# Optimization experiments

Measured on AMD Instinct MI355X. Metric: run time of the kernel, lower is better.

Reference implementation:

```python
import jax, jax.numpy as jnp
import numpy as np

NUM_HEADS = 16
NEG = -1e9


def setup_inputs() -> dict:
    key = jax.random.key(0)
    ks = jax.random.split(key, 16)
    B, Sq, Skv, E = 4, 4096, 4096, 1024
    scale = 1.0 / np.sqrt(E)
    inp = {
        "q": jax.random.normal(ks[0], (B, Sq, E), jnp.float32),
        "k": jax.random.normal(ks[1], (B, Skv, E), jnp.float32),
        "v": jax.random.normal(ks[2], (B, Skv, E), jnp.float32),
        "q_padding_mask": jax.random.randint(ks[3], (B, Sq, 1), 0, 2).astype(bool),
        "key_padding_mask": jax.random.randint(ks[4], (B, Skv, 1), 0, 2).astype(bool),
        "Wq": jax.random.normal(ks[5], (E, E), jnp.float32) * scale,
        "bq": jnp.zeros((E,), jnp.float32),
        "Wk": jax.random.normal(ks[6], (E, E), jnp.float32) * scale,
        "bk": jnp.zeros((E,), jnp.float32),
        "Wv": jax.random.normal(ks[7], (E, E), jnp.float32) * scale,
        "bv": jnp.zeros((E,), jnp.float32),
        "Wp": jax.random.normal(ks[8], (E, E), jnp.float32) * scale,
        "bp": jnp.zeros((E,), jnp.float32),
    }
    return inp


def _split_heads(x, H):
    B, S, E = x.shape
    return x.reshape(B, S, H, E // H).transpose(0, 2, 1, 3)  # (B,H,S,D)


def reference(q, k, v, q_padding_mask, key_padding_mask, Wq, bq, Wk, bk, Wv, bv, Wp, bp):
    B, Sq, E = q.shape
    H = NUM_HEADS
    # padding: q*mask + ~mask*(-1e9) == where(mask, q, -1e9)
    q = jnp.where(q_padding_mask, q, NEG)
    k = jnp.where(key_padding_mask, k, NEG)
    v = v * key_padding_mask
    # projections (torch nn.Linear: x @ W.T + b)
    qh = _split_heads(q @ Wq.T + bq, H)  # (B,H,Sq,D)
    kh = _split_heads(k @ Wk.T + bk, H)  # (B,H,Skv,D)
    vh = _split_heads(v @ Wv.T + bv, H)  # (B,H,Skv,D)
    qh = jax.nn.softmax(qh, axis=-1)
    kh = jax.nn.softmax(kh, axis=-1)
    k_cumsum = kh.sum(axis=-2, keepdims=True)              # (B,H,1,D)
    a_t = 1.0 / (qh * k_cumsum).sum(axis=-1, keepdims=True)  # (B,H,Sq,1)
    context = jnp.einsum("bhsd,bhse->bhde", kh, vh)        # (B,H,D,D)
    out = jnp.einsum("bhqd,bhde->bhqe", qh, context) * a_t + qh
    out = out.transpose(0, 2, 1, 3).reshape(B, Sq, E)
    out = out @ Wp.T + bp
    return out * q_padding_mask
```

## Files before the change

### kernel.cpp

```cpp
#include <hip/hip_runtime.h>
#include <hip/hip_bf16.h>
#include <stdint.h>


typedef __bf16 bf16_t;
typedef __bf16 v8bf __attribute__((ext_vector_type(8)));
typedef __bf16 v4bf __attribute__((ext_vector_type(4)));
typedef float  v4f  __attribute__((ext_vector_type(4)));

#define NSPLIT 16

__device__ __forceinline__ void gl_lds16(const void* g, void* l) {
  __builtin_amdgcn_global_load_lds((const __attribute__((address_space(1))) void*)g,
                                   (__attribute__((address_space(3))) void*)l,
                                   16, 0, 0);
}

__global__ __launch_bounds__(256) void convert_w(
    const float* __restrict__ W0, const float* __restrict__ W1,
    const float* __restrict__ W2, const float* __restrict__ W3,
    bf16_t* __restrict__ dst)
{
  int g = blockIdx.x * 256 + threadIdx.x;
  int seg = g >> 17;
  int off = (g & 131071) * 8;
  const float* s = (seg == 0 ? W0 : seg == 1 ? W1 : seg == 2 ? W2 : W3) + off;
  v4f a = *(const v4f*)s, b = *(const v4f*)(s + 4);
  v8bf o;
#pragma unroll
  for (int j = 0; j < 4; j++) { o[j] = (bf16_t)a[j]; o[4 + j] = (bf16_t)b[j]; }
  *(v8bf*)(dst + (size_t)seg * 1048576 + off) = o;
}

__device__ __forceinline__ void cvt_chunk(const float* __restrict__ s,
                                          bf16_t* __restrict__ d, size_t chunk)
{
  const size_t i = chunk * 8;
  v4f a = *(const v4f*)(s + i), b = *(const v4f*)(s + i + 4);
  v8bf o;
#pragma unroll
  for (int j = 0; j < 4; j++) { o[j] = (bf16_t)a[j]; o[4 + j] = (bf16_t)b[j]; }
  *(v8bf*)(d + i) = o;
}

__global__ __launch_bounds__(256) void convert_kv_kernel(
    const float* __restrict__ k, const float* __restrict__ v,
    bf16_t* __restrict__ kb, bf16_t* __restrict__ vb)
{
  const size_t t = (size_t)blockIdx.x * 256 + threadIdx.x;
#pragma unroll
  for (int j = 0; j < 4; j++) cvt_chunk(k, kb, t + (size_t)j * 524288);
#pragma unroll
  for (int j = 0; j < 4; j++) cvt_chunk(v, vb, t + (size_t)j * 524288);
}

__global__ __launch_bounds__(256) void convert_q_kernel(
    const float* __restrict__ q, bf16_t* __restrict__ qb)
{
  const size_t t = (size_t)blockIdx.x * 256 + threadIdx.x;
#pragma unroll
  for (int j = 0; j < 4; j++) cvt_chunk(q, qb, t + (size_t)j * 524288);
}

__global__ __launch_bounds__(256) void rowsum_kernel(
    const float* __restrict__ Wq, const float* __restrict__ bq,
    const float* __restrict__ Wk, const float* __restrict__ bk,
    float* __restrict__ rs)
{
  int w = threadIdx.x >> 6, l = threadIdx.x & 63;
  int row = blockIdx.x * 4 + w;
  int r = (row < 1024) ? row : row - 1024;
  const float* W = ((row < 1024) ? Wq : Wk) + (size_t)r * 1024 + l * 16;
  float s = 0.f;
#pragma unroll
  for (int i = 0; i < 4; i++) {
    v4f x = *(const v4f*)(W + i * 4);
    s += x[0] + x[1] + x[2] + x[3];
  }
#pragma unroll
  for (int sh = 1; sh < 64; sh <<= 1) s += __shfl_xor(s, sh, 64);
  if (l == 0) {
    float b = (row < 1024) ? bq[r] : bk[r];
    rs[row] = -1e9f * s + b;
  }
}

template <int EPI>
__global__ __launch_bounds__(512, 2) void gemm_bt(
    const bf16_t* __restrict__ A, const bf16_t* __restrict__ Wb,
    const float* __restrict__ bias, const int* __restrict__ rowmask,
    const float* __restrict__ rs, void* __restrict__ Cout)
{
  constexpr int K = 1024, N = 1024;
  constexpr int NT = 16;
  __shared__ __align__(16) bf16_t As[2][256 * 64];
  __shared__ __align__(16) bf16_t Bs[2][256 * 64];
  const int t = threadIdx.x;
  const int l = t & 63;
  const int w = t >> 6;
  const int wm = w >> 2, wn = w & 3;
  const int xcd = blockIdx.x & 7, seq = blockIdx.x >> 3;
  const int by = xcd * 8 + (seq & 7), bx = seq >> 3;
  const int m0 = by << 8, n0 = bx << 8;

  const int srow = t >> 3;
  const int sgs  = (t & 7) ^ (srow & 7);
  const bf16_t* Ag = A  + (size_t)(m0 + srow) * K + sgs * 8;
  const bf16_t* Bg = Wb + (size_t)(n0 + srow) * K + sgs * 8;
  bf16_t* lA = &As[0][0] + t * 8;
  bf16_t* lB = &Bs[0][0] + t * 8;

  auto stageA = [&](int half, int kt, int buf) {
    const bf16_t* s = Ag + (size_t)(half * 128) * K + (kt << 6);
    bf16_t* d = lA + buf * 16384 + half * 8192;
    gl_lds16(s, d);
    gl_lds16(s + (size_t)64 * K, d + 4096);
  };
  auto stageB = [&](int half, int kt, int buf) {
    const bf16_t* s = Bg + (size_t)(half * 128) * K + (kt << 6);
    bf16_t* d = lB + buf * 16384 + half * 8192;
    gl_lds16(s, d);
    gl_lds16(s + (size_t)64 * K, d + 4096);
  };

  const int lr = l & 15, kg = l >> 4;
  const int xg0 = ((kg)     ^ (lr & 7)) * 8;
  const int xg1 = ((4 + kg) ^ (lr & 7)) * 8;
  const int aB = (wm * 128 + lr) * 64;
  const int bB = (wn * 64  + lr) * 64;

  v4f acc[8][4] = {};
  v8bf bfr[4][2];

#define QUAD(R0, R1, A0_, A1_, A2_, A3_)                                        \
  {                                                                             \
    __builtin_amdgcn_s_setprio(1);                                              \
    _Pragma("unroll")                                                           \
    for (int c = 0; c < 4; ++c) {                                               \
      acc[R0][c] = __builtin_amdgcn_mfma_f32_16x16x32_bf16(A0_, bfr[c][0], acc[R0][c], 0, 0, 0); \
      acc[R0][c] = __builtin_amdgcn_mfma_f32_16x16x32_bf16(A1_, bfr[c][1], acc[R0][c], 0, 0, 0); \
      acc[R1][c] = __builtin_amdgcn_mfma_f32_16x16x32_bf16(A2_, bfr[c][0], acc[R1][c], 0, 0, 0); \
      acc[R1][c] = __builtin_amdgcn_mfma_f32_16x16x32_bf16(A3_, bfr[c][1], acc[R1][c], 0, 0, 0); \
    }                                                                           \
    __builtin_amdgcn_s_setprio(0);                                              \
  }

  stageA(0, 0, 0); stageA(1, 0, 0); stageB(0, 0, 0); stageB(1, 0, 0);
  stageB(0, 1, 1); stageB(1, 1, 1);
  asm volatile("s_waitcnt vmcnt(4)" ::: "memory");
  __builtin_amdgcn_s_barrier();

  for (int s = 0; s < NT; ++s) {
    const int b = s & 1;
    const bf16_t* Ab = &As[b][0];
    const bf16_t* Bb = &Bs[b][0];
    v8bf a0, a1, a2, a3;
#pragma unroll
    for (int c = 0; c < 4; ++c) {
      bfr[c][0] = *(const v8bf*)(Bb + bB + c * 1024 + xg0);
      bfr[c][1] = *(const v8bf*)(Bb + bB + c * 1024 + xg1);
    }
    a0 = *(const v8bf*)(Ab + aB + 0 * 1024 + xg0);
    a1 = *(const v8bf*)(Ab + aB + 0 * 1024 + xg1);
    a2 = *(const v8bf*)(Ab + aB + 1 * 1024 + xg0);
    a3 = *(const v8bf*)(Ab + aB + 1 * 1024 + xg1);
    if (s + 1 < NT) { stageA(0, s + 1, b ^ 1); stageA(1, s + 1, b ^ 1); }
    __builtin_amdgcn_s_barrier();
    QUAD(0, 1, a0, a1, a2, a3);
    __builtin_amdgcn_s_barrier();
    a0 = *(const v8bf*)(Ab + aB + 2 * 1024 + xg0);
    a1 = *(const v8bf*)(Ab + aB + 2 * 1024 + xg1);
    a2 = *(const v8bf*)(Ab + aB + 3 * 1024 + xg0);
    a3 = *(const v8bf*)(Ab + aB + 3 * 1024 + xg1);
    __builtin_amdgcn_s_barrier();
    QUAD(2, 3, a0, a1, a2, a3);
    __builtin_amdgcn_s_barrier();
    a0 = *(const v8bf*)(Ab + aB + 4 * 1024 + xg0);
    a1 = *(const v8bf*)(Ab + aB + 4 * 1024 + xg1);
    a2 = *(const v8bf*)(Ab + aB + 5 * 1024 + xg0);
    a3 = *(const v8bf*)(Ab + aB + 5 * 1024 + xg1);
    if (s + 2 < NT) { stageB(0, s + 2, b); stageB(1, s + 2, b); }
    __builtin_amdgcn_s_barrier();
    QUAD(4, 5, a0, a1, a2, a3);
    __builtin_amdgcn_s_barrier();
    a0 = *(const v8bf*)(Ab + aB + 6 * 1024 + xg0);
    a1 = *(const v8bf*)(Ab + aB + 6 * 1024 + xg1);
    a2 = *(const v8bf*)(Ab + aB + 7 * 1024 + xg0);
    a3 = *(const v8bf*)(Ab + aB + 7 * 1024 + xg1);
    __builtin_amdgcn_s_barrier();
    QUAD(6, 7, a0, a1, a2, a3);
    if (s < NT - 2) asm volatile("s_waitcnt vmcnt(4)" ::: "memory");
    else            asm volatile("s_waitcnt vmcnt(0)" ::: "memory");
    __builtin_amdgcn_s_barrier();
  }
#undef QUAD

  const int rq = kg * 4;
  float bcol[4], rscol[4]; int colg[4];
#pragma unroll
  for (int c = 0; c < 4; c++) {
    colg[c] = n0 + wn * 64 + c * 16 + lr;
    bcol[c] = bias[colg[c]];
    rscol[c] = (EPI == 1) ? rs[colg[c]] : 0.f;
  }
#pragma unroll
  for (int r = 0; r < 8; r++) {
    int rowBase = m0 + wm * 128 + r * 16 + rq;
#pragma unroll
    for (int i = 0; i < 4; i++) {
      int row = rowBase + i;
      int msk = rowmask[row];
      float vv[4];
#pragma unroll
      for (int c = 0; c < 4; c++) {
        float x = acc[r][c][i] + bcol[c];
        if (EPI == 0)      x = msk ? x : bcol[c];
        else if (EPI == 1) x = msk ? x : rscol[c];
        else               x = msk ? x : 0.f;
        vv[c] = x;
      }
      if (EPI == 1) {
        float mx = fmaxf(fmaxf(vv[0], vv[1]), fmaxf(vv[2], vv[3]));
#pragma unroll
        for (int sh = 1; sh < 16; sh <<= 1) mx = fmaxf(mx, __shfl_xor(mx, sh, 64));
        float e0 = __expf(vv[0] - mx), e1 = __expf(vv[1] - mx);
        float e2 = __expf(vv[2] - mx), e3 = __expf(vv[3] - mx);
        float sum = e0 + e1 + e2 + e3;
#pragma unroll
        for (int sh = 1; sh < 16; sh <<= 1) sum += __shfl_xor(sum, sh, 64);
        float rinv = 1.0f / sum;
        vv[0] = e0 * rinv; vv[1] = e1 * rinv; vv[2] = e2 * rinv; vv[3] = e3 * rinv;
      }
#pragma unroll
      for (int c = 0; c < 4; c++) {
        size_t idx = (size_t)row * N + colg[c];
        if (EPI == 2) ((float*)Cout)[idx] = vv[c];
        else          ((bf16_t*)Cout)[idx] = (bf16_t)vv[c];
      }
    }
  }
}

__global__ __launch_bounds__(256) void ctx_partial(
    const bf16_t* __restrict__ kh, const bf16_t* __restrict__ vh,
    float* __restrict__ ctx, float* __restrict__ kc)
{
  __shared__ __align__(16) float khTf[2][64][36];
  __shared__ __align__(16) float vhTf[2][64][36];
  const int bh = blockIdx.x & 63;
  const int sp = blockIdx.x >> 6;
  const int b = bh >> 4, h = bh & 15;
  const int t = threadIdx.x;
  const int l = t & 63;
  const int w = t >> 6;
  const int wm = w >> 1, wn = w & 1;

  const int a  = t & 7;
  const int d0 = a * 8;
  const int sl = t >> 3;
  const int sw = sl ^ (a << 2);

  const size_t base = ((size_t)b * 4096) * 1024 + h * 64;
  const int sBeg = sp * (4096 / NSPLIT);
  const int nch = (4096 / NSPLIT) / 32;
  const bf16_t* kp = kh + base + (size_t)(sBeg + sl) * 1024 + d0;
  const bf16_t* vp = vh + base + (size_t)(sBeg + sl) * 1024 + d0;

  const int lr = l & 15;
  const int gl = l >> 4;

  v8bf ones;
#pragma unroll
  for (int j = 0; j < 8; j++) ones[j] = (bf16_t)1.0f;

  v4f acc[2][2] = {};
  v4f kca[2] = {};

  auto loadfrag = [&](const float (*T)[36], int rowbase) -> v8bf {
    const int row = rowbase + lr;
    const float* rp = &T[row][0];
    const int g0 = ((gl << 1) ^ (row >> 3)) & 7;
    v4f pa = *(const v4f*)(rp + g0 * 4);
    v4f pb = *(const v4f*)(rp + (g0 ^ 1) * 4);
    v8bf f;
#pragma unroll
    for (int j = 0; j < 4; j++) { f[j] = (bf16_t)pa[j]; f[4 + j] = (bf16_t)pb[j]; }
    return f;
  };

  v8bf rk = *(const v8bf*)kp;
  v8bf rv = *(const v8bf*)vp;
  for (int c = 0; c < nch; c++) {
    const int cur = c & 1;
#pragma unroll
    for (int j = 0; j < 8; j++) {
      khTf[cur][d0 + j][sw] = (float)rk[j];
      vhTf[cur][d0 + j][sw] = (float)rv[j];
    }
    if (c + 1 < nch) {
      rk = *(const v8bf*)(kp + (size_t)(c + 1) * 32 * 1024);
      rv = *(const v8bf*)(vp + (size_t)(c + 1) * 32 * 1024);
    }
    __syncthreads();
    v8bf af0 = loadfrag(khTf[cur], wm * 32);
    v8bf af1 = loadfrag(khTf[cur], wm * 32 + 16);
    v8bf bf0 = loadfrag(vhTf[cur], wn * 32);
    v8bf bf1 = loadfrag(vhTf[cur], wn * 32 + 16);
    acc[0][0] = __builtin_amdgcn_mfma_f32_16x16x32_bf16(af0, bf0, acc[0][0], 0, 0, 0);
    acc[0][1] = __builtin_amdgcn_mfma_f32_16x16x32_bf16(af0, bf1, acc[0][1], 0, 0, 0);
    acc[1][0] = __builtin_amdgcn_mfma_f32_16x16x32_bf16(af1, bf0, acc[1][0], 0, 0, 0);
    acc[1][1] = __builtin_amdgcn_mfma_f32_16x16x32_bf16(af1, bf1, acc[1][1], 0, 0, 0);
    if (wn == 0) {
      kca[0] = __builtin_amdgcn_mfma_f32_16x16x32_bf16(af0, ones, kca[0], 0, 0, 0);
      kca[1] = __builtin_amdgcn_mfma_f32_16x16x32_bf16(af1, ones, kca[1], 0, 0, 0);
    }
    __syncthreads();
  }

  const int rq = gl * 4;
  float* cp = ctx + (size_t)bh * 4096;
#pragma unroll
  for (int r = 0; r < 2; r++)
#pragma unroll
    for (int cc = 0; cc < 2; cc++) {
      const int e = wn * 32 + cc * 16 + lr;
#pragma unroll
      for (int i = 0; i < 4; i++) {
        const int d = wm * 32 + r * 16 + rq + i;
        atomicAdd(&cp[d * 64 + e], acc[r][cc][i]);
      }
    }
  if (wn == 0 && lr == 0) {
#pragma unroll
    for (int r = 0; r < 2; r++)
#pragma unroll
      for (int i = 0; i < 4; i++) {
        const int d = wm * 32 + r * 16 + rq + i;
        atomicAdd(&kc[bh * 64 + d], kca[r][i]);
      }
  }
}

__global__ __launch_bounds__(256) void outpre_kernel(
    const bf16_t* __restrict__ qh, const float* __restrict__ ctx,
    const float* __restrict__ kc, bf16_t* __restrict__ outp)
{
  __shared__ __align__(16) bf16_t qs[128][66];
  __shared__ __align__(16) float ctxs[64][64];
  __shared__ float kcs[64];
  const int blk = blockIdx.x;
  const int st = blk & 31, h = (blk >> 5) & 15, b = blk >> 9;
  const int bh = b * 16 + h;
  const int t = threadIdx.x;
  const int s0 = st * 128;
  const size_t base = ((size_t)b * 4096 + s0) * 1024 + h * 64;

  {
    const int row = t >> 1, half = t & 1;
    const bf16_t* src = qh + base + (size_t)row * 1024 + half * 32;
#pragma unroll
    for (int j = 0; j < 4; j++) {
      v8bf qv = *(const v8bf*)(src + j * 8);
      uint32_t wv[4];
      __builtin_memcpy(wv, &qv, 16);
      uint32_t* pw = (uint32_t*)&qs[row][half * 32 + j * 8];
      pw[0] = wv[0]; pw[1] = wv[1]; pw[2] = wv[2]; pw[3] = wv[3];
    }
  }
  const float* cg = ctx + (size_t)bh * 4096;
#pragma unroll
  for (int i = 0; i < 4; i++) {
    int off = i * 1024 + t * 4;
    *(v4f*)((float*)ctxs + off) = *(const v4f*)(cg + off);
  }
  if (t < 64) kcs[t] = kc[bh * 64 + t];
  __syncthreads();

  const int er = t & 3, e0 = er * 16;
  const int rp = t >> 2;
  const int r0 = rp * 2;
  float at[2] = {};
  float acc[2][16] = {};
  for (int d = 0; d < 64; d++) {
    const float kcd = kcs[d];
    const float q0 = (float)qs[r0][d];
    const float q1 = (float)qs[r0 + 1][d];
    at[0] += q0 * kcd;
    at[1] += q1 * kcd;
    const float* cr = &ctxs[d][e0];
    v4f ca = *(const v4f*)cr,        cb = *(const v4f*)(cr + 4);
    v4f cc3 = *(const v4f*)(cr + 8), cd4 = *(const v4f*)(cr + 12);
#pragma unroll
    for (int i = 0; i < 4; i++) {
      acc[0][i]      += q0 * ca[i];   acc[1][i]      += q1 * ca[i];
      acc[0][4 + i]  += q0 * cb[i];   acc[1][4 + i]  += q1 * cb[i];
      acc[0][8 + i]  += q0 * cc3[i];  acc[1][8 + i]  += q1 * cc3[i];
      acc[0][12 + i] += q0 * cd4[i];  acc[1][12 + i] += q1 * cd4[i];
    }
  }
#pragma unroll
  for (int j = 0; j < 2; j++) {
    const int row = r0 + j;
    const float rinv = 1.0f / at[j];
    bf16_t* op = outp + base + (size_t)row * 1024 + e0;
    v8bf o0, o1;
#pragma unroll
    for (int i = 0; i < 8; i++) {
      o0[i] = (bf16_t)(acc[j][i] * rinv + (float)qs[row][e0 + i]);
      o1[i] = (bf16_t)(acc[j][8 + i] * rinv + (float)qs[row][e0 + 8 + i]);
    }
    *(v8bf*)op = o0;
    *(v8bf*)(op + 8) = o1;
  }
}

extern "C" void kernel_launch(void* const* d_in, const int* in_sizes, int n_in,
                              void* d_out, int out_size, void* d_ws, size_t ws_size,
                              hipStream_t stream)
{
  const float* q  = (const float*)d_in[0];
  const float* k  = (const float*)d_in[1];
  const float* v  = (const float*)d_in[2];
  const int* qmask = (const int*)d_in[3];
  const int* kmask = (const int*)d_in[4];
  const float* Wq = (const float*)d_in[5];
  const float* bq = (const float*)d_in[6];
  const float* Wk = (const float*)d_in[7];
  const float* bk = (const float*)d_in[8];
  const float* Wv = (const float*)d_in[9];
  const float* bv = (const float*)d_in[10];
  const float* Wp = (const float*)d_in[11];
  const float* bp = (const float*)d_in[12];

  const int M = 16384;
  char* ws = (char*)d_ws;
  size_t off = 0;
  auto alloc = [&](size_t bytes) {
    void* p = ws + off; off += (bytes + 255) & ~(size_t)255; return p;
  };
  bf16_t* wb   = (bf16_t*)alloc(4 * 1048576 * 2);
  bf16_t* abuf = (bf16_t*)alloc((size_t)M * 1024 * 2);
  float* ctx   = (float*)alloc((64 * 4096 + 64 * 64) * 4);
  float* kc    = ctx + 64 * 4096;
  float* rs    = (float*)alloc(2048 * 4);
  bf16_t* Wqb = wb, *Wkb = wb + 1048576, *Wvb = wb + 2097152, *Wpb = wb + 3145728;
  bf16_t* lo = (bf16_t*)d_out;
  bf16_t* hi = (bf16_t*)((char*)d_out + 33554432);

  hipMemsetAsync(ctx, 0, (64 * 4096 + 64 * 64) * 4, stream);
  convert_w<<<2048, 256, 0, stream>>>(Wq, Wk, Wv, Wp, wb);
  rowsum_kernel<<<512, 256, 0, stream>>>(Wq, bq, Wk, bk, rs);
  convert_kv_kernel<<<2048, 256, 0, stream>>>(k, v, lo, hi);

  const int gblocks = (M / 256) * (1024 / 256);
  gemm_bt<1><<<gblocks, 512, 0, stream>>>(lo, Wkb, bk, kmask, rs + 1024, abuf);
  gemm_bt<0><<<gblocks, 512, 0, stream>>>(hi, Wvb, bv, kmask, nullptr, lo);
  ctx_partial<<<64 * NSPLIT, 256, 0, stream>>>(abuf, lo, ctx, kc);
  convert_q_kernel<<<2048, 256, 0, stream>>>(q, hi);
  gemm_bt<1><<<gblocks, 512, 0, stream>>>(hi, Wqb, bq, qmask, rs, abuf);
  outpre_kernel<<<2048, 256, 0, stream>>>(abuf, ctx, kc, abuf);
  gemm_bt<2><<<gblocks, 512, 0, stream>>>(abuf, Wpb, bp, qmask, nullptr, d_out);
}
```

Baseline: 469.5 us.

## Fuse fp32-to-bf16 input conversion into GEMM A-tile loading

```diff
diff --git a/kernel.cpp b/kernel.cpp
--- a/kernel.cpp
+++ b/kernel.cpp
@@ -32,36 +32,6 @@
   *(v8bf*)(dst + (size_t)seg * 1048576 + off) = o;
 }
 
-__device__ __forceinline__ void cvt_chunk(const float* __restrict__ s,
-                                          bf16_t* __restrict__ d, size_t chunk)
-{
-  const size_t i = chunk * 8;
-  v4f a = *(const v4f*)(s + i), b = *(const v4f*)(s + i + 4);
-  v8bf o;
-#pragma unroll
-  for (int j = 0; j < 4; j++) { o[j] = (bf16_t)a[j]; o[4 + j] = (bf16_t)b[j]; }
-  *(v8bf*)(d + i) = o;
-}
-
-__global__ __launch_bounds__(256) void convert_kv_kernel(
-    const float* __restrict__ k, const float* __restrict__ v,
-    bf16_t* __restrict__ kb, bf16_t* __restrict__ vb)
-{
-  const size_t t = (size_t)blockIdx.x * 256 + threadIdx.x;
-#pragma unroll
-  for (int j = 0; j < 4; j++) cvt_chunk(k, kb, t + (size_t)j * 524288);
-#pragma unroll
-  for (int j = 0; j < 4; j++) cvt_chunk(v, vb, t + (size_t)j * 524288);
-}
-
-__global__ __launch_bounds__(256) void convert_q_kernel(
-    const float* __restrict__ q, bf16_t* __restrict__ qb)
-{
-  const size_t t = (size_t)blockIdx.x * 256 + threadIdx.x;
-#pragma unroll
-  for (int j = 0; j < 4; j++) cvt_chunk(q, qb, t + (size_t)j * 524288);
-}
-
 __global__ __launch_bounds__(256) void rowsum_kernel(
     const float* __restrict__ Wq, const float* __restrict__ bq,
     const float* __restrict__ Wk, const float* __restrict__ bk,
@@ -85,9 +55,9 @@
   }
 }
 
-template <int EPI>
+template <int EPI, int AF32>
 __global__ __launch_bounds__(512, 2) void gemm_bt(
-    const bf16_t* __restrict__ A, const bf16_t* __restrict__ Wb,
+    const void* __restrict__ Ax, const bf16_t* __restrict__ Wb,
     const float* __restrict__ bias, const int* __restrict__ rowmask,
     const float* __restrict__ rs, void* __restrict__ Cout)
 {
@@ -105,7 +75,8 @@
 
   const int srow = t >> 3;
   const int sgs  = (t & 7) ^ (srow & 7);
-  const bf16_t* Ag = A  + (size_t)(m0 + srow) * K + sgs * 8;
+  const bf16_t* Ag = (const bf16_t*)Ax + (size_t)(m0 + srow) * K + sgs * 8;
+  const float*  Af = (const float*) Ax + (size_t)(m0 + srow) * K + sgs * 8;
   const bf16_t* Bg = Wb + (size_t)(n0 + srow) * K + sgs * 8;
   bf16_t* lA = &As[0][0] + t * 8;
   bf16_t* lB = &Bs[0][0] + t * 8;
@@ -121,6 +92,28 @@
     bf16_t* d = lB + buf * 16384 + half * 8192;
     gl_lds16(s, d);
     gl_lds16(s + (size_t)64 * K, d + 4096);
+  };
+
+  v4f ald[4][2];
+  auto issueA = [&](int kt) {
+#pragma unroll
+    for (int r = 0; r < 4; r++) {
+      const float* p = Af + (size_t)(r * 64) * K + (kt << 6);
+      ald[r][0] = *(const v4f*)p;
+      ald[r][1] = *(const v4f*)(p + 4);
+    }
+  };
+  auto writeA = [&](int buf) {
+#pragma unroll
+    for (int r = 0; r < 4; r++) {
+      v8bf o;
+#pragma unroll
+      for (int j = 0; j < 4; j++) {
+        o[j]     = (bf16_t)ald[r][0][j];
+        o[4 + j] = (bf16_t)ald[r][1][j];
+      }
+      *(v8bf*)(lA + buf * 16384 + r * 4096) = o;
+    }
   };
 
   const int lr = l & 15, kg = l >> 4;
@@ -145,9 +138,13 @@
     __builtin_amdgcn_s_setprio(0);                                              \
   }
 
-  stageA(0, 0, 0); stageA(1, 0, 0); stageB(0, 0, 0); stageB(1, 0, 0);
+  if (AF32) issueA(0);
+  else { stageA(0, 0, 0); stageA(1, 0, 0); }
+  stageB(0, 0, 0); stageB(1, 0, 0);
   stageB(0, 1, 1); stageB(1, 1, 1);
+  if (AF32) writeA(0);
   asm volatile("s_waitcnt vmcnt(4)" ::: "memory");
+  asm volatile("s_waitcnt lgkmcnt(0)" ::: "memory");
   __builtin_amdgcn_s_barrier();
 
   for (int s = 0; s < NT; ++s) {
@@ -155,6 +152,10 @@
     const bf16_t* Ab = &As[b][0];
     const bf16_t* Bb = &Bs[b][0];
     v8bf a0, a1, a2, a3;
+    if (s + 1 < NT) {
+      if (AF32) issueA(s + 1);
+      else { stageA(0, s + 1, b ^ 1); stageA(1, s + 1, b ^ 1); }
+    }
 #pragma unroll
     for (int c = 0; c < 4; ++c) {
       bfr[c][0] = *(const v8bf*)(Bb + bB + c * 1024 + xg0);
@@ -164,7 +165,6 @@
     a1 = *(const v8bf*)(Ab + aB + 0 * 1024 + xg1);
     a2 = *(const v8bf*)(Ab + aB + 1 * 1024 + xg0);
     a3 = *(const v8bf*)(Ab + aB + 1 * 1024 + xg1);
-    if (s + 1 < NT) { stageA(0, s + 1, b ^ 1); stageA(1, s + 1, b ^ 1); }
     __builtin_amdgcn_s_barrier();
     QUAD(0, 1, a0, a1, a2, a3);
     __builtin_amdgcn_s_barrier();
@@ -189,8 +189,10 @@
     a3 = *(const v8bf*)(Ab + aB + 7 * 1024 + xg1);
     __builtin_amdgcn_s_barrier();
     QUAD(6, 7, a0, a1, a2, a3);
+    if (AF32 && s + 1 < NT) writeA(b ^ 1);
     if (s < NT - 2) asm volatile("s_waitcnt vmcnt(4)" ::: "memory");
     else            asm volatile("s_waitcnt vmcnt(0)" ::: "memory");
+    asm volatile("s_waitcnt lgkmcnt(0)" ::: "memory");
     __builtin_amdgcn_s_barrier();
   }
 #undef QUAD
@@ -445,19 +447,16 @@
   float* rs    = (float*)alloc(2048 * 4);
   bf16_t* Wqb = wb, *Wkb = wb + 1048576, *Wvb = wb + 2097152, *Wpb = wb + 3145728;
   bf16_t* lo = (bf16_t*)d_out;
-  bf16_t* hi = (bf16_t*)((char*)d_out + 33554432);
 
   hipMemsetAsync(ctx, 0, (64 * 4096 + 64 * 64) * 4, stream);
   convert_w<<<2048, 256, 0, stream>>>(Wq, Wk, Wv, Wp, wb);
   rowsum_kernel<<<512, 256, 0, stream>>>(Wq, bq, Wk, bk, rs);
-  convert_kv_kernel<<<2048, 256, 0, stream>>>(k, v, lo, hi);
 
   const int gblocks = (M / 256) * (1024 / 256);
-  gemm_bt<1><<<gblocks, 512, 0, stream>>>(lo, Wkb, bk, kmask, rs + 1024, abuf);
-  gemm_bt<0><<<gblocks, 512, 0, stream>>>(hi, Wvb, bv, kmask, nullptr, lo);
+  gemm_bt<1, 1><<<gblocks, 512, 0, stream>>>(k, Wkb, bk, kmask, rs + 1024, abuf);
+  gemm_bt<0, 1><<<gblocks, 512, 0, stream>>>(v, Wvb, bv, kmask, nullptr, lo);
   ctx_partial<<<64 * NSPLIT, 256, 0, stream>>>(abuf, lo, ctx, kc);
-  convert_q_kernel<<<2048, 256, 0, stream>>>(q, hi);
-  gemm_bt<1><<<gblocks, 512, 0, stream>>>(hi, Wqb, bq, qmask, rs, abuf);
+  gemm_bt<1, 1><<<gblocks, 512, 0, stream>>>(q, Wqb, bq, qmask, rs, abuf);
   outpre_kernel<<<2048, 256, 0, stream>>>(abuf, ctx, kc, abuf);
-  gemm_bt<2><<<gblocks, 512, 0, stream>>>(abuf, Wpb, bp, qmask, nullptr, d_out);
-}
+  gemm_bt<2, 0><<<gblocks, 512, 0, stream>>>(abuf, Wpb, bp, qmask, nullptr, d_out);
+}
```

After: 436.0 us. 1.08x faster.
